# Performance work log

Measured on AMD Instinct MI355X. Metric: run time of the kernel, lower is better.

Reference implementation:

```python
import jax, jax.numpy as jnp
import numpy as np

B, XD, ZD, XE, H, NH = 8192, 4096, 1024, 64, 128, 4
NUM_STEPS, STEP, NOISE = 10, 0.01, 1.0
EPS = 1e-5


def setup_inputs() -> dict:
    key = jax.random.key(0)
    ks = jax.random.split(key, 16)
    w = lambda k, s: jax.random.normal(k, s, jnp.float32) * 0.02
    inp = {"x": jax.random.normal(ks[0], (B, XD), jnp.float32)}
    inp.update(
        px_W1=w(ks[1], (H, ZD)), px_b1=jnp.zeros(H, jnp.float32),
        px_W2=w(ks[2], (XD, H)), px_b2=jnp.zeros(XD, jnp.float32),
        emb_W=w(ks[3], (XE, XD)), emb_b=jnp.zeros(XE, jnp.float32),
        xp_W=w(ks[4], (H, XE)), xp_b=jnp.zeros(H, jnp.float32),
        zp_W=w(ks[5], (H, ZD)), zp_b=jnp.zeros(H, jnp.float32),
        sa_Wqkv=w(ks[6], (3 * H, H)), sa_bqkv=jnp.zeros(3 * H, jnp.float32),
        sa_Wo=w(ks[7], (H, H)), sa_bo=jnp.zeros(H, jnp.float32),
        ca_Wqkv=w(ks[8], (3 * H, H)), ca_bqkv=jnp.zeros(3 * H, jnp.float32),
        ca_Wo=w(ks[9], (H, H)), ca_bo=jnp.zeros(H, jnp.float32),
        ffn_W1=w(ks[10], (H, H)), ffn_b1=jnp.zeros(H, jnp.float32),
        ffn_W2=w(ks[11], (H, H)), ffn_b2=jnp.zeros(H, jnp.float32),
        ln1_g=jnp.ones(H, jnp.float32), ln1_b=jnp.zeros(H, jnp.float32),
        ln2_g=jnp.ones(H, jnp.float32), ln2_b=jnp.zeros(H, jnp.float32),
        ln3_g=jnp.ones(H, jnp.float32), ln3_b=jnp.zeros(H, jnp.float32),
        out_W=w(ks[12], (1, H)), out_b=jnp.zeros(1, jnp.float32),
    )
    return inp


def _ln(x, g, b):
    m = jnp.mean(x, -1, keepdims=True)
    v = jnp.var(x, -1, keepdims=True)
    return (x - m) * jax.lax.rsqrt(v + EPS) * g + b


def _mha(q, k, v, Wqkv, bqkv, Wo, bo):
    # torch nn.MultiheadAttention math, batch-first layout (B, S, E)
    E = q.shape[-1]
    d = E // NH
    Wq, Wk, Wv = jnp.split(Wqkv, 3, 0)
    bq, bk, bv = jnp.split(bqkv, 3, 0)
    hd = lambda t, W, bb: (t @ W.T + bb).reshape(t.shape[0], t.shape[1], NH, d)
    qh, kh, vh = hd(q, Wq, bq), hd(k, Wk, bk), hd(v, Wv, bv)
    s = jnp.einsum('bqhd,bkhd->bhqk', qh, kh) / jnp.sqrt(jnp.float32(d))
    a = jax.nn.softmax(s, -1)
    o = jnp.einsum('bhqk,bkhd->bqhd', a, vh).reshape(q.shape[0], q.shape[1], E)
    return o @ Wo.T + bo


def _forward(x, px_W1, px_b1, px_W2, px_b2, emb_W, emb_b, xp_W, xp_b, zp_W, zp_b,
             sa_Wqkv, sa_bqkv, sa_Wo, sa_bo, ca_Wqkv, ca_bqkv, ca_Wo, ca_bo,
             ffn_W1, ffn_b1, ffn_W2, ffn_b2, ln1_g, ln1_b, ln2_g, ln2_b,
             ln3_g, ln3_b, out_W, out_b):
    bsz = x.shape[0]
    px = lambda z: jax.nn.relu(z @ px_W1.T + px_b1) @ px_W2.T + px_b2
    grad_fn = jax.grad(lambda z: jnp.sum((px(z) - x) ** 2))
    ks = jax.random.split(jax.random.key(42), NUM_STEPS + 1)
    z0 = jax.random.normal(ks[0], (bsz, ZD), jnp.float32)

    def step(z, k):
        z = z - 0.5 * STEP * grad_fn(z)
        z = z + NOISE * jnp.sqrt(jnp.float32(STEP)) * jax.random.normal(k, z.shape, z.dtype)
        return z, None

    z, _ = jax.lax.scan(step, z0, ks[1:])
    z = jax.lax.stop_gradient(z)  # torch: z.detach()

    x_recon = px(z)                               # (B, XD)
    x_tok = (x @ emb_W.T + emb_b)[:, None, :]     # (B, 1, XE)
    z_lat = z[:, None, :]                         # (B, 1, ZD)
    x_h = x_tok @ xp_W.T + xp_b                   # (B, 1, H)
    z_h = z_lat @ zp_W.T + zp_b                   # (B, 1, H)
    sa = _mha(x_h, x_h, x_h, sa_Wqkv, sa_bqkv, sa_Wo, sa_bo)
    h1 = _ln(x_h + sa, ln1_g, ln1_b)
    ca = _mha(h1, z_h, z_h, ca_Wqkv, ca_bqkv, ca_Wo, ca_bo)
    h2 = _ln(h1 + ca, ln2_g, ln2_b)
    ff = jax.nn.relu(h2 @ ffn_W1.T + ffn_b1) @ ffn_W2.T + ffn_b2
    h3 = _ln(h2 + ff, ln3_g, ln3_b)
    y_pred = h3 @ out_W.T + out_b                 # (B, 1, 1)
    return x_recon, y_pred


def reference(x, px_W1, px_b1, px_W2, px_b2, emb_W, emb_b, xp_W, xp_b, zp_W, zp_b,
              sa_Wqkv, sa_bqkv, sa_Wo, sa_bo, ca_Wqkv, ca_bqkv, ca_Wo, ca_bo,
              ffn_W1, ffn_b1, ffn_W2, ffn_b2, ln1_g, ln1_b, ln2_g, ln2_b,
              ln3_g, ln3_b, out_W, out_b):
    return _forward(x, px_W1, px_b1, px_W2, px_b2, emb_W, emb_b, xp_W, xp_b,
                    zp_W, zp_b, sa_Wqkv, sa_bqkv, sa_Wo, sa_bo, ca_Wqkv,
                    ca_bqkv, ca_Wo, ca_bo, ffn_W1, ffn_b1, ffn_W2, ffn_b2,
                    ln1_g, ln1_b, ln2_g, ln2_b, ln3_g, ln3_b, out_W, out_b)
```

## Files before the change

kernel.cpp:

```cpp
#include <hip/hip_runtime.h>
#include <hip/hip_bf16.h>
#include <cstdint>
#include <cstddef>
#include <cmath>

#define B_     8192
#define XD_    4096
#define ZD_    1024
#define XE_    64
#define H_     128
#define ZN_    (B_*ZD_)

typedef __attribute__((ext_vector_type(8))) short short8_t;
typedef __attribute__((ext_vector_type(4))) float f32x4_t;
#define MFMA16(a,b,c) __builtin_amdgcn_mfma_f32_16x16x32_bf16((a),(b),(c),0,0,0)

__host__ __device__ __forceinline__ uint32_t rotl32_(uint32_t x, int r){ return (x<<r)|(x>>(32-r)); }

__host__ __device__ __forceinline__ void tf2x32(uint32_t k0, uint32_t k1,
                                                uint32_t x0, uint32_t x1,
                                                uint32_t* o0, uint32_t* o1){
  uint32_t k2 = k0 ^ k1 ^ 0x1BD11BDAu;
  x0 += k0; x1 += k1;
  x0 += x1; x1 = rotl32_(x1,13); x1 ^= x0;
  x0 += x1; x1 = rotl32_(x1,15); x1 ^= x0;
  x0 += x1; x1 = rotl32_(x1,26); x1 ^= x0;
  x0 += x1; x1 = rotl32_(x1, 6); x1 ^= x0;
  x0 += k1; x1 += k2 + 1u;
  x0 += x1; x1 = rotl32_(x1,17); x1 ^= x0;
  x0 += x1; x1 = rotl32_(x1,29); x1 ^= x0;
  x0 += x1; x1 = rotl32_(x1,16); x1 ^= x0;
  x0 += x1; x1 = rotl32_(x1,24); x1 ^= x0;
  x0 += k2; x1 += k0 + 2u;
  x0 += x1; x1 = rotl32_(x1,13); x1 ^= x0;
  x0 += x1; x1 = rotl32_(x1,15); x1 ^= x0;
  x0 += x1; x1 = rotl32_(x1,26); x1 ^= x0;
  x0 += x1; x1 = rotl32_(x1, 6); x1 ^= x0;
  x0 += k0; x1 += k1 + 3u;
  x0 += x1; x1 = rotl32_(x1,17); x1 ^= x0;
  x0 += x1; x1 = rotl32_(x1,29); x1 ^= x0;
  x0 += x1; x1 = rotl32_(x1,16); x1 ^= x0;
  x0 += x1; x1 = rotl32_(x1,24); x1 ^= x0;
  x0 += k1; x1 += k2 + 4u;
  x0 += x1; x1 = rotl32_(x1,13); x1 ^= x0;
  x0 += x1; x1 = rotl32_(x1,15); x1 ^= x0;
  x0 += x1; x1 = rotl32_(x1,26); x1 ^= x0;
  x0 += x1; x1 = rotl32_(x1, 6); x1 ^= x0;
  x0 += k2; x1 += k0 + 5u;
  *o0 = x0; *o1 = x1;
}

__device__ __forceinline__ float erfinv_(float x){
  float w = -__logf(fmaf(-x, x, 1.0f));
  float p;
  if (w < 5.0f){
    w -= 2.5f;
    p = 2.81022636e-08f;
    p = fmaf(p, w, 3.43273939e-07f);
    p = fmaf(p, w, -3.5233877e-06f);
    p = fmaf(p, w, -4.39150654e-06f);
    p = fmaf(p, w, 0.00021858087f);
    p = fmaf(p, w, -0.00125372503f);
    p = fmaf(p, w, -0.00417768164f);
    p = fmaf(p, w, 0.246640727f);
    p = fmaf(p, w, 1.50140941f);
  } else {
    w = sqrtf(w) - 3.0f;
    p = -0.000200214257f;
    p = fmaf(p, w, 0.000100950558f);
    p = fmaf(p, w, 0.00134934322f);
    p = fmaf(p, w, -0.00367342844f);
    p = fmaf(p, w, 0.00573950773f);
    p = fmaf(p, w, -0.0076224613f);
    p = fmaf(p, w, 0.00943887047f);
    p = fmaf(p, w, 1.00167406f);
    p = fmaf(p, w, 2.83297682f);
  }
  return p * x;
}

__device__ __forceinline__ float bits_to_normal(uint32_t bits){
  float f = __uint_as_float((bits >> 9) | 0x3f800000u) - 1.0f;
  float u = fmaxf(-0.99999994f, fmaf(f, 2.0f, -0.99999994f));
  return 1.41421356f * erfinv_(u);
}

__device__ __forceinline__ float rng_normal(uint32_t k0, uint32_t k1, uint32_t idx){
  uint32_t o0, o1; tf2x32(k0, k1, 0u, idx, &o0, &o1);
  return bits_to_normal(o0 ^ o1);
}

__device__ __forceinline__ ushort f2bf(float f){
  return __builtin_bit_cast(ushort, __float2bfloat16(f));
}
__device__ __forceinline__ float bf2f(ushort u){ return __uint_as_float(((uint32_t)u) << 16); }

__global__ void k_prepA(const float* __restrict__ saWo, const float* __restrict__ saWqkv,
                        const float* __restrict__ caWo, const float* __restrict__ caWqkv,
                        float* __restrict__ S, float* __restrict__ U){
  int blk = blockIdx.x, tid = threadIdx.x;
  int idx = (blk & 255) * 64 + tid;
  int i = idx >> 7, j = idx & 127;
  if (blk < 256){
    float acc = (i == j) ? 1.0f : 0.0f;
    for (int k = 0; k < H_; ++k) acc += saWo[i*H_ + k] * saWqkv[(2*H_ + k)*H_ + j];
    S[idx] = acc;
  } else {
    float acc = 0.0f;
    for (int k = 0; k < H_; ++k) acc += caWo[i*H_ + k] * caWqkv[(2*H_ + k)*H_ + j];
    U[idx] = acc;
  }
}

__global__ void k_prepB(const float* __restrict__ saWo, const float* __restrict__ sabqkv, const float* __restrict__ sabo,
                        const float* __restrict__ caWo, const float* __restrict__ cabqkv, const float* __restrict__ cabo,
                        const float* __restrict__ W2, const float* __restrict__ pb2,
                        float* __restrict__ s0, float* __restrict__ u0, float* __restrict__ cb,
                        uint32_t* __restrict__ dkeys){
  int blk = blockIdx.x, tid = threadIdx.x;
  if (blk == 0 && tid == 0){
    for (uint32_t i = 0; i < 11; ++i){
      uint32_t a, b; tf2x32(0u, 42u, 0u, i, &a, &b);
      dkeys[2*i] = a; dkeys[2*i+1] = b;
    }
  }
  if (blk < 2){
    int i = blk*64 + tid;
    float acc = sabo[i];
    for (int k = 0; k < H_; ++k) acc += saWo[i*H_ + k] * sabqkv[2*H_ + k];
    s0[i] = acc;
  } else if (blk < 4){
    int i = (blk-2)*64 + tid;
    float acc = cabo[i];
    for (int k = 0; k < H_; ++k) acc += caWo[i*H_ + k] * cabqkv[2*H_ + k];
    u0[i] = acc;
  } else {
    int j = (blk-4)*64 + tid;
    float acc = 0.0f;
    for (int c = 0; c < XD_; ++c) acc += pb2[c] * W2[(size_t)c*H_ + j];
    cb[j] = acc;
  }
}

__global__ void k_prepM(const float* __restrict__ W2, float* __restrict__ M){
  int idx = blockIdx.x*64 + threadIdx.x;
  int j1 = idx >> 7, j2 = idx & 127;
  float acc = 0.0f;
  for (int c = 0; c < XD_; ++c) acc += W2[(size_t)c*H_ + j1] * W2[(size_t)c*H_ + j2];
  M[idx] = acc;
}

__global__ void k_prepTR(const float* __restrict__ S, const float* __restrict__ U,
                         const float* __restrict__ xpW, const float* __restrict__ zpW,
                         const float* __restrict__ xpb, const float* __restrict__ zpb,
                         const float* __restrict__ s0, const float* __restrict__ u0,
                         float* __restrict__ T, float* __restrict__ R,
                         float* __restrict__ t0, float* __restrict__ r0v){
  int blk = blockIdx.x, tid = threadIdx.x;
  if (blk < 128){
    int idx = blk*64 + tid;
    int i = idx >> 6, e = idx & 63;
    float acc = 0.0f;
    for (int m = 0; m < H_; ++m) acc += S[i*H_ + m] * xpW[m*XE_ + e];
    T[idx] = acc;
  } else if (blk < 2176){
    int idx = (blk-128)*64 + tid;
    int i = idx >> 10, k = idx & 1023;
    float acc = 0.0f;
    for (int m = 0; m < H_; ++m) acc += U[i*H_ + m] * zpW[(size_t)m*ZD_ + k];
    R[idx] = acc;
  } else if (blk < 2178){
    int i = (blk-2176)*64 + tid;
    float acc = s0[i];
    for (int m = 0; m < H_; ++m) acc += S[i*H_ + m] * xpb[m];
    t0[i] = acc;
  } else {
    int i = (blk-2178)*64 + tid;
    float acc = u0[i];
    for (int m = 0; m < H_; ++m) acc += U[i*H_ + m] * zpb[m];
    r0v[i] = acc;
  }
}

__global__ void k_prepWXT(const float* __restrict__ W2, const float* __restrict__ T,
                          const float* __restrict__ embW, const float* __restrict__ embb,
                          const float* __restrict__ t0,
                          ushort* __restrict__ WXT, float* __restrict__ q0){
  int idx = blockIdx.x*256 + threadIdx.x;
  int j = idx >> 12, c = idx & 4095;
  float v;
  if (j < H_) v = W2[(size_t)c*H_ + j];
  else {
    int i = j - H_;
    float acc = 0.0f;
    for (int e = 0; e < XE_; ++e) acc += T[i*XE_ + e] * embW[(size_t)e*XD_ + c];
    v = acc;
  }
  WXT[idx] = f2bf(v);
  if (idx < H_){
    float acc = t0[idx];
    for (int e = 0; e < XE_; ++e) acc += T[idx*XE_ + e] * embb[e];
    q0[idx] = acc;
  }
}

__global__ void k_conv(const float* __restrict__ W2, const float* __restrict__ W1,
                       const float* __restrict__ Mm, const float* __restrict__ R,
                       ushort* __restrict__ W2bf, ushort* __restrict__ Mbf,
                       ushort* __restrict__ FBT){
  int idx = blockIdx.x*256 + threadIdx.x;
  if (idx < 524288) W2bf[idx] = f2bf(W2[idx]);
  else if (idx < 540672){ int i = idx - 524288; Mbf[i] = f2bf(2.0f*Mm[i]); }
  else { int i = idx - 540672; int j = i >> 10, k = i & 1023;
    FBT[i] = f2bf(j < H_ ? W1[j*ZD_ + k] : R[(size_t)(j-H_)*ZD_ + k]); }
}

__global__ void k_prepG(const float* __restrict__ W1, const float* __restrict__ R,
                        ushort* __restrict__ GGr){
  int idx = blockIdx.x*64 + threadIdx.x;
  int i = idx >> 7, k = idx & 127;
  float acc = 0.0f;
  if (i < 128){
    for (int m = 0; m < ZD_; ++m) acc += W1[(size_t)i*ZD_ + m] * W1[(size_t)k*ZD_ + m];
  } else {
    for (int m = 0; m < ZD_; ++m) acc += W1[(size_t)k*ZD_ + m] * R[(size_t)(i-128)*ZD_ + m];
  }
  GGr[idx] = f2bf(-0.005f * acc);
}

__global__ __launch_bounds__(256) void k_xpass_mfma(
    const float* __restrict__ x, const ushort* __restrict__ WXT,
    const float* __restrict__ cb, const float* __restrict__ q0,
    float* __restrict__ cneg, float* __restrict__ h1pre){
  __shared__ __align__(16) ushort xt[2][32*72];
  __shared__ __align__(16) ushort bt[2][128*72];
  const int t = threadIdx.x, lane = t & 63, w = t >> 6;
  const int bm = blockIdx.x >> 1, bn = blockIdx.x & 1;
  const int row0 = bm*32, ncol0 = bn*128;
  const int l15 = lane & 15, kq8 = (lane >> 4)*8, rq = (lane >> 4)*4;
  const int rt = w & 1, cb4 = (w >> 1)*4;
  const int xr = t >> 3, xk = (t & 7)*8;
  const int wn = t >> 1, wk = (t & 1)*32;
  f32x4_t acc[4] = {};
  {
    float4 v0 = *(const float4*)&x[(size_t)(row0+xr)*XD_ + xk];
    float4 v1 = *(const float4*)&x[(size_t)(row0+xr)*XD_ + xk + 4];
    union { ushort u[8]; uint4 q; } p;
    p.u[0]=f2bf(v0.x); p.u[1]=f2bf(v0.y); p.u[2]=f2bf(v0.z); p.u[3]=f2bf(v0.w);
    p.u[4]=f2bf(v1.x); p.u[5]=f2bf(v1.y); p.u[6]=f2bf(v1.z); p.u[7]=f2bf(v1.w);
    *(uint4*)&xt[0][xr*72 + xk] = p.q;
    const ushort* s = &WXT[(size_t)(ncol0+wn)*XD_ + wk];
    uint4 b0v=*(const uint4*)s, b1v=*(const uint4*)(s+8), b2v=*(const uint4*)(s+16), b3v=*(const uint4*)(s+24);
    ushort* d = &bt[0][wn*72 + wk];
    *(uint4*)d=b0v; *(uint4*)(d+8)=b1v; *(uint4*)(d+16)=b2v; *(uint4*)(d+24)=b3v;
  }
  float4 xv0, xv1; uint4 wb0, wb1, wb2, wb3;
  {
    xv0 = *(const float4*)&x[(size_t)(row0+xr)*XD_ + 64 + xk];
    xv1 = *(const float4*)&x[(size_t)(row0+xr)*XD_ + 64 + xk + 4];
    const ushort* s = &WXT[(size_t)(ncol0+wn)*XD_ + 64 + wk];
    wb0=*(const uint4*)s; wb1=*(const uint4*)(s+8); wb2=*(const uint4*)(s+16); wb3=*(const uint4*)(s+24);
  }
  #pragma unroll 1
  for (int it = 0; it < 64; ++it){
    __syncthreads();
    if (it < 63){
      union { ushort u[8]; uint4 q; } p;
      p.u[0]=f2bf(xv0.x); p.u[1]=f2bf(xv0.y); p.u[2]=f2bf(xv0.z); p.u[3]=f2bf(xv0.w);
      p.u[4]=f2bf(xv1.x); p.u[5]=f2bf(xv1.y); p.u[6]=f2bf(xv1.z); p.u[7]=f2bf(xv1.w);
      *(uint4*)&xt[(it+1)&1][xr*72 + xk] = p.q;
      ushort* d = &bt[(it+1)&1][wn*72 + wk];
      *(uint4*)d=wb0; *(uint4*)(d+8)=wb1; *(uint4*)(d+16)=wb2; *(uint4*)(d+24)=wb3;
    }
    if (it < 62){
      const int kt = (it+2)*64;
      xv0 = *(const float4*)&x[(size_t)(row0+xr)*XD_ + kt + xk];
      xv1 = *(const float4*)&x[(size_t)(row0+xr)*XD_ + kt + xk + 4];
      const ushort* s = &WXT[(size_t)(ncol0+wn)*XD_ + kt + wk];
      wb0=*(const uint4*)s; wb1=*(const uint4*)(s+8); wb2=*(const uint4*)(s+16); wb3=*(const uint4*)(s+24);
    }
    const ushort* xb = &xt[it&1][(rt*16+l15)*72];
    const ushort* bb = &bt[it&1][0];
    #pragma unroll
    for (int h = 0; h < 2; ++h){
      short8_t a = *(const short8_t*)(xb + h*32 + kq8);
      #pragma unroll
      for (int c = 0; c < 4; ++c){
        short8_t b = *(const short8_t*)(bb + ((cb4+c)*16+l15)*72 + h*32 + kq8);
        acc[c] = MFMA16(a, b, acc[c]);
      }
    }
  }
  #pragma unroll
  for (int c = 0; c < 4; ++c){
    int jl = (cb4+c)*16 + l15;
    #pragma unroll
    for (int r = 0; r < 4; ++r){
      int row = row0 + rt*16 + rq + r;
      float v = acc[c][r];
      if (bn == 0) cneg[(size_t)row*H_ + jl] = 2.0f*(cb[jl] - v);
      else         h1pre[(size_t)row*H_ + jl] = v + q0[jl];
    }
  }
}

__global__ __launch_bounds__(256) void k_noiseproj(
    const ushort* __restrict__ FBT, const uint32_t* __restrict__ dkeys,
    float* __restrict__ y0c0, ushort* __restrict__ NWR){
  __shared__ __align__(16) ushort at[64*72];
  const int t = threadIdx.x, lane = t & 63, w = t >> 6;
  const int l15 = lane & 15, kq8 = (lane >> 4)*8, rq = (lane >> 4)*4;
  const int p = blockIdx.x >> 7, mb = blockIdx.x & 127;
  const int gb0 = mb*64;
  const uint32_t k0 = dkeys[2*p], k1 = dkeys[2*p+1];
  const int arow = t >> 2, ak0 = (t & 3)*16;
  f32x4_t acc[16] = {};
  #pragma unroll 1
  for (int it = 0; it < 16; ++it){
    __syncthreads();
    {
      uint32_t base = (uint32_t)(gb0 + arow)*1024u + (uint32_t)(it*64 + ak0);
      union { ushort u[8]; uint4 q; } pk;
      #pragma unroll
      for (int j = 0; j < 8; ++j) pk.u[j] = f2bf(rng_normal(k0,k1,base+j));
      *(uint4*)&at[arow*72 + ak0] = pk.q;
      #pragma unroll
      for (int j = 0; j < 8; ++j) pk.u[j] = f2bf(rng_normal(k0,k1,base+8+j));
      *(uint4*)&at[arow*72 + ak0 + 8] = pk.q;
    }
    __syncthreads();
    #pragma unroll
    for (int h = 0; h < 2; ++h){
      short8_t a = *(const short8_t*)&at[(w*16+l15)*72 + h*32 + kq8];
      #pragma unroll
      for (int cf = 0; cf < 16; ++cf){
        short8_t b = *(const short8_t*)&FBT[(size_t)(cf*16+l15)*ZD_ + it*64 + h*32 + kq8];
        acc[cf] = MFMA16(a, b, acc[cf]);
      }
    }
  }
  #pragma unroll
  for (int cf = 0; cf < 16; ++cf){
    int col = cf*16 + l15;
    #pragma unroll
    for (int r = 0; r < 4; ++r){
      int row = gb0 + w*16 + rq + r;
      float v = acc[cf][r];
      if (p == 0) y0c0[(size_t)row*256 + col] = v;
      else NWR[(size_t)(p-1)*2097152 + (size_t)row*256 + col] = f2bf(0.1f*v);
    }
  }
}

__global__ __launch_bounds__(512) void k_lv2(
    const ushort* __restrict__ M2bf, const ushort* __restrict__ GGr,
    const float* __restrict__ y0c0, const ushort* __restrict__ NWR,
    const float* __restrict__ b1, const float* __restrict__ r0v,
    const float* __restrict__ cneg,
    ushort* __restrict__ hfin_bf, float* __restrict__ capre){
  __shared__ __align__(16) ushort abuf[16*136];
  __shared__ __align__(16) ushort glbuf[16*136];
  const int t = threadIdx.x, lane = t & 63, w = t >> 6;
  const int l15 = lane & 15, kq8 = (lane >> 4)*8, rq = (lane >> 4)*4;
  const int b0 = blockIdx.x * 16;
  const int myc = w*16 + l15;
  const int col2 = w*32 + l15;

  f32x4_t acc[2];
  #pragma unroll
  for (int nf = 0; nf < 2; ++nf)
    #pragma unroll
    for (int r = 0; r < 4; ++r)
      acc[nf][r] = y0c0[(size_t)(b0+rq+r)*256 + col2 + nf*16];
  float cn[4];
  #pragma unroll
  for (int r = 0; r < 4; ++r) cn[r] = cneg[(size_t)(b0+rq+r)*H_ + myc];
  float bb2[2];
  bb2[0] = (w < 4) ? b1[col2] : 0.0f;
  bb2[1] = (w < 4) ? b1[col2+16] : 0.0f;
  ushort nx[8];
  #pragma unroll
  for (int nf = 0; nf < 2; ++nf)
    #pragma unroll
    for (int r = 0; r < 4; ++r)
      nx[nf*4+r] = NWR[(size_t)(b0+rq+r)*256 + col2 + nf*16];

  #pragma unroll 1
  for (int s = 0; s < 10; ++s){
    if (w < 4){
      #pragma unroll
      for (int nf = 0; nf < 2; ++nf)
        #pragma unroll
        for (int r = 0; r < 4; ++r)
          abuf[(rq+r)*136 + col2 + nf*16] = f2bf(fmaxf(acc[nf][r] + bb2[nf], 0.0f));
    }
    __syncthreads();
    f32x4_t g2 = {};
    #pragma unroll
    for (int h = 0; h < 4; ++h){
      short8_t a = *(const short8_t*)&abuf[l15*136 + h*32 + kq8];
      short8_t b = *(const short8_t*)&M2bf[(size_t)myc*H_ + h*32 + kq8];
      g2 = MFMA16(a, b, g2);
// ... 145 lines not shown
  }
  x0 = h2a + fa; x1 = h2b + fbv;
  m = wsum64(x0 + x1) * (1.0f/128.0f);
  d0 = x0 - m; d1 = x1 - m;
  v = wsum64(d0*d0 + d1*d1) * (1.0f/128.0f);
  rs = rsqrtf(v + 1e-5f);
  float h3a = d0 * rs * ln3g[l]    + ln3b[l];
  float h3b = d1 * rs * ln3g[l+64] + ln3b[l+64];
  float py = wsum64(outW[l]*h3a + outW[l+64]*h3b);
  if (l == 0) y[b] = py + outb[0];
}

extern "C" void kernel_launch(void* const* d_in, const int* in_sizes, int n_in,
                              void* d_out, int out_size, void* d_ws, size_t ws_size,
                              hipStream_t stream){
  const float* x      = (const float*)d_in[0];
  const float* pxW1   = (const float*)d_in[1];
  const float* pxb1   = (const float*)d_in[2];
  const float* pxW2   = (const float*)d_in[3];
  const float* pxb2   = (const float*)d_in[4];
  const float* embW   = (const float*)d_in[5];
  const float* embb   = (const float*)d_in[6];
  const float* xpW    = (const float*)d_in[7];
  const float* xpb    = (const float*)d_in[8];
  const float* zpW    = (const float*)d_in[9];
  const float* zpb    = (const float*)d_in[10];
  const float* saWqkv = (const float*)d_in[11];
  const float* sabqkv = (const float*)d_in[12];
  const float* saWo   = (const float*)d_in[13];
  const float* sabo   = (const float*)d_in[14];
  const float* caWqkv = (const float*)d_in[15];
  const float* cabqkv = (const float*)d_in[16];
  const float* caWo   = (const float*)d_in[17];
  const float* cabo   = (const float*)d_in[18];
  const float* fW1    = (const float*)d_in[19];
  const float* fb1    = (const float*)d_in[20];
  const float* fW2    = (const float*)d_in[21];
  const float* fb2    = (const float*)d_in[22];
  const float* ln1g   = (const float*)d_in[23];
  const float* ln1b   = (const float*)d_in[24];
  const float* ln2g   = (const float*)d_in[25];
  const float* ln2b   = (const float*)d_in[26];
  const float* ln3g   = (const float*)d_in[27];
  const float* ln3b   = (const float*)d_in[28];
  const float* outW   = (const float*)d_in[29];
  const float* outb   = (const float*)d_in[30];
  (void)in_sizes; (void)n_in; (void)out_size; (void)ws_size;

  float* ws    = (float*)d_ws;
  float* cneg  = ws;
  float* h1pre = cneg + (size_t)B_*H_;
  float* capre = h1pre + (size_t)B_*H_;
  float* Rm    = capre + (size_t)B_*H_;
  float* Mm    = Rm + (size_t)H_*ZD_;
  float* Sm    = Mm + H_*H_;
  float* Um    = Sm + H_*H_;
  float* Tm    = Um + H_*H_;
  float* vs0   = Tm + H_*XE_;
  float* vu0   = vs0 + H_;
  float* vt0   = vu0 + H_;
  float* vq0   = vt0 + H_;
  float* vr0   = vq0 + H_;
  float* vcb   = vr0 + H_;
  uint32_t* dkeys = (uint32_t*)(vcb + H_);
  float* y0c0  = (float*)(dkeys + 32);
  ushort* WXT   = (ushort*)(y0c0 + (size_t)B_*256);
  ushort* W2bf  = WXT + (size_t)256*XD_;
  ushort* Mbf   = W2bf + (size_t)XD_*H_;
  ushort* FBT   = Mbf + H_*H_;
  ushort* GGr   = FBT + (size_t)256*ZD_;
  ushort* hfin  = GGr + (size_t)256*H_;
  ushort* NWR   = hfin + (size_t)B_*H_;

  float* xre   = (float*)d_out;
  float* ypred = xre + (size_t)B_*XD_;

  k_prepA   <<<512,  64, 0, stream>>>(saWo, saWqkv, caWo, caWqkv, Sm, Um);
  k_prepB   <<<6,    64, 0, stream>>>(saWo, sabqkv, sabo, caWo, cabqkv, cabo, pxW2, pxb2,
                                      vs0, vu0, vcb, dkeys);
  k_prepM   <<<256,  64, 0, stream>>>(pxW2, Mm);
  k_prepTR  <<<2180, 64, 0, stream>>>(Sm, Um, xpW, zpW, xpb, zpb, vs0, vu0, Tm, Rm, vt0, vr0);
  k_prepWXT <<<4096, 256, 0, stream>>>(pxW2, Tm, embW, embb, vt0, WXT, vq0);
  k_conv    <<<3136, 256, 0, stream>>>(pxW2, pxW1, Mm, Rm, W2bf, Mbf, FBT);
  k_prepG   <<<512,  64, 0, stream>>>(pxW1, Rm, GGr);
  k_noiseproj <<<1408, 256, 0, stream>>>(FBT, dkeys, y0c0, NWR);
  k_xpass_mfma <<<512, 256, 0, stream>>>(x, WXT, vcb, vq0, cneg, h1pre);
  k_lv2     <<<512, 512, 0, stream>>>(Mbf, GGr, y0c0, NWR, pxb1, vr0, cneg, hfin, capre);
  k_xrecon_mfma <<<4096, 256, 0, stream>>>(hfin, W2bf, pxb2, xre);
  k_tail    <<<2048, 256, 0, stream>>>(h1pre, capre, ln1g, ln1b, ln2g, ln2b, ln3g, ln3b,
                                       fW1, fb1, fW2, fb2, outW, outb, ypred);
}
```

Before: 900.2 us.

## Merge noise projection and x-pass GEMMs into one interleaved kernel

Two kernels are fused into one launch: the compute-bound RNG noise-projection GEMM and the memory-bound x-projection GEMM. Blocks are interleaved 11:4 so both kinds of work share the GPU at once and overlap. The noise-projection path also gets a double-buffered LDS tile, so the next RNG tile is generated while MFMAs run on the current one. The cost is a larger shared buffer for the noise blocks (sized for the x-pass), which may lower occupancy, plus higher register pressure from holding prefetched RNG values.

```diff
diff --git a/kernel.cpp b/kernel.cpp
--- a/kernel.cpp
+++ b/kernel.cpp
@@ -95,6 +95,14 @@
 }
 __device__ __forceinline__ float bf2f(ushort u){ return __uint_as_float(((uint32_t)u) << 16); }
 
+__device__ __forceinline__ void gen16(uint32_t k0, uint32_t k1, uint32_t base,
+                                      uint4* g0, uint4* g1){
+  union { ushort u[16]; uint4 q[2]; } pk;
+  #pragma unroll
+  for (int j = 0; j < 16; ++j) pk.u[j] = f2bf(rng_normal(k0,k1,base+(uint32_t)j));
+  *g0 = pk.q[0]; *g1 = pk.q[1];
+}
+
 __global__ void k_prepA(const float* __restrict__ saWo, const float* __restrict__ saWqkv,
                         const float* __restrict__ caWo, const float* __restrict__ caWqkv,
                         float* __restrict__ S, float* __restrict__ U){
@@ -228,126 +236,132 @@
   GGr[idx] = f2bf(-0.005f * acc);
 }
 
-__global__ __launch_bounds__(256) void k_xpass_mfma(
+__global__ __launch_bounds__(256) void k_npx(
+    const ushort* __restrict__ FBT, const uint32_t* __restrict__ dkeys,
+    float* __restrict__ y0c0, ushort* __restrict__ NWR,
     const float* __restrict__ x, const ushort* __restrict__ WXT,
-    const float* __restrict__ cb, const float* __restrict__ q0,
+    const float* __restrict__ cb, const float* __restrict__ q0v,
     float* __restrict__ cneg, float* __restrict__ h1pre){
-  __shared__ __align__(16) ushort xt[2][32*72];
-  __shared__ __align__(16) ushort bt[2][128*72];
-  const int t = threadIdx.x, lane = t & 63, w = t >> 6;
-  const int bm = blockIdx.x >> 1, bn = blockIdx.x & 1;
-  const int row0 = bm*32, ncol0 = bn*128;
-  const int l15 = lane & 15, kq8 = (lane >> 4)*8, rq = (lane >> 4)*4;
-  const int rt = w & 1, cb4 = (w >> 1)*4;
-  const int xr = t >> 3, xk = (t & 7)*8;
-  const int wn = t >> 1, wk = (t & 1)*32;
-  f32x4_t acc[4] = {};
-  {
-    float4 v0 = *(const float4*)&x[(size_t)(row0+xr)*XD_ + xk];
-    float4 v1 = *(const float4*)&x[(size_t)(row0+xr)*XD_ + xk + 4];
-    union { ushort u[8]; uint4 q; } p;
-    p.u[0]=f2bf(v0.x); p.u[1]=f2bf(v0.y); p.u[2]=f2bf(v0.z); p.u[3]=f2bf(v0.w);
-    p.u[4]=f2bf(v1.x); p.u[5]=f2bf(v1.y); p.u[6]=f2bf(v1.z); p.u[7]=f2bf(v1.w);
-    *(uint4*)&xt[0][xr*72 + xk] = p.q;
-    const ushort* s = &WXT[(size_t)(ncol0+wn)*XD_ + wk];
-    uint4 b0v=*(const uint4*)s, b1v=*(const uint4*)(s+8), b2v=*(const uint4*)(s+16), b3v=*(const uint4*)(s+24);
-    ushort* d = &bt[0][wn*72 + wk];
-    *(uint4*)d=b0v; *(uint4*)(d+8)=b1v; *(uint4*)(d+16)=b2v; *(uint4*)(d+24)=b3v;
-  }
-  float4 xv0, xv1; uint4 wb0, wb1, wb2, wb3;
-  {
-    xv0 = *(const float4*)&x[(size_t)(row0+xr)*XD_ + 64 + xk];
-    xv1 = *(const float4*)&x[(size_t)(row0+xr)*XD_ + 64 + xk + 4];
-    const ushort* s = &WXT[(size_t)(ncol0+wn)*XD_ + 64 + wk];
-    wb0=*(const uint4*)s; wb1=*(const uint4*)(s+8); wb2=*(const uint4*)(s+16); wb3=*(const uint4*)(s+24);
-  }
-  #pragma unroll 1
-  for (int it = 0; it < 64; ++it){
-    __syncthreads();
-    if (it < 63){
-      union { ushort u[8]; uint4 q; } p;
-      p.u[0]=f2bf(xv0.x); p.u[1]=f2bf(xv0.y); p.u[2]=f2bf(xv0.z); p.u[3]=f2bf(xv0.w);
-      p.u[4]=f2bf(xv1.x); p.u[5]=f2bf(xv1.y); p.u[6]=f2bf(xv1.z); p.u[7]=f2bf(xv1.w);
-      *(uint4*)&xt[(it+1)&1][xr*72 + xk] = p.q;
-      ushort* d = &bt[(it+1)&1][wn*72 + wk];
-      *(uint4*)d=wb0; *(uint4*)(d+8)=wb1; *(uint4*)(d+16)=wb2; *(uint4*)(d+24)=wb3;
-    }
-    if (it < 62){
-      const int kt = (it+2)*64;
-      xv0 = *(const float4*)&x[(size_t)(row0+xr)*XD_ + kt + xk];
-      xv1 = *(const float4*)&x[(size_t)(row0+xr)*XD_ + kt + xk + 4];
-      const ushort* s = &WXT[(size_t)(ncol0+wn)*XD_ + kt + wk];
-      wb0=*(const uint4*)s; wb1=*(const uint4*)(s+8); wb2=*(const uint4*)(s+16); wb3=*(const uint4*)(s+24);
-    }
-    const ushort* xb = &xt[it&1][(rt*16+l15)*72];
-    const ushort* bb = &bt[it&1][0];
-    #pragma unroll
-    for (int h = 0; h < 2; ++h){
-      short8_t a = *(const short8_t*)(xb + h*32 + kq8);
-      #pragma unroll
-      for (int c = 0; c < 4; ++c){
-        short8_t b = *(const short8_t*)(bb + ((cb4+c)*16+l15)*72 + h*32 + kq8);
-        acc[c] = MFMA16(a, b, acc[c]);
-      }
-    }
-  }
-  #pragma unroll
-  for (int c = 0; c < 4; ++c){
-    int jl = (cb4+c)*16 + l15;
-    #pragma unroll
-    for (int r = 0; r < 4; ++r){
-      int row = row0 + rt*16 + rq + r;
-      float v = acc[c][r];
-      if (bn == 0) cneg[(size_t)row*H_ + jl] = 2.0f*(cb[jl] - v);
-      else         h1pre[(size_t)row*H_ + jl] = v + q0[jl];
-    }
-  }
-}
-
-__global__ __launch_bounds__(256) void k_noiseproj(
-    const ushort* __restrict__ FBT, const uint32_t* __restrict__ dkeys,
-    float* __restrict__ y0c0, ushort* __restrict__ NWR){
-  __shared__ __align__(16) ushort at[64*72];
+  __shared__ __align__(16) ushort smem[23040];
   const int t = threadIdx.x, lane = t & 63, w = t >> 6;
   const int l15 = lane & 15, kq8 = (lane >> 4)*8, rq = (lane >> 4)*4;
-  const int p = blockIdx.x >> 7, mb = blockIdx.x & 127;
-  const int gb0 = mb*64;
-  const uint32_t k0 = dkeys[2*p], k1 = dkeys[2*p+1];
-  const int arow = t >> 2, ak0 = (t & 3)*16;
-  f32x4_t acc[16] = {};
-  #pragma unroll 1
-  for (int it = 0; it < 16; ++it){
+  const int grp = blockIdx.x / 15, rem = blockIdx.x % 15;
+
+  if (rem < 11){
+    ushort* at0 = smem;
+    ushort* at1 = smem + 4608;
+    const int np = grp*11 + rem;
+    const int p = np >> 7, mb = np & 127;
+    const int gb0 = mb*64;
+    const uint32_t k0 = dkeys[2*p], k1 = dkeys[2*p+1];
+    const int arow = t >> 2, ak0 = (t & 3)*16;
+    const uint32_t rbase = (uint32_t)(gb0 + arow)*1024u + (uint32_t)ak0;
+    f32x4_t acc[16] = {};
+    uint4 g0, g1;
+    gen16(k0, k1, rbase, &g0, &g1);
+    { ushort* d = at0 + arow*72 + ak0; *(uint4*)d = g0; *(uint4*)(d+8) = g1; }
     __syncthreads();
+    #pragma unroll 1
+    for (int it = 0; it < 16; ++it){
+      if (it < 15) gen16(k0, k1, rbase + (uint32_t)((it+1)*64), &g0, &g1);
+      const ushort* ab = ((it & 1) ? at1 : at0) + (w*16 + l15)*72;
+      #pragma unroll
+      for (int h = 0; h < 2; ++h){
+        short8_t a = *(const short8_t*)(ab + h*32 + kq8);
+        #pragma unroll
+        for (int cf = 0; cf < 16; ++cf){
+          short8_t b = *(const short8_t*)&FBT[(size_t)(cf*16+l15)*ZD_ + it*64 + h*32 + kq8];
+          acc[cf] = MFMA16(a, b, acc[cf]);
+        }
+      }
+      if (it < 15){
+        ushort* d = ((it & 1) ? at0 : at1) + arow*72 + ak0;
+        *(uint4*)d = g0; *(uint4*)(d+8) = g1;
+      }
+      __syncthreads();
+    }
+    #pragma unroll
+    for (int cf = 0; cf < 16; ++cf){
+      int col = cf*16 + l15;
+      #pragma unroll
+      for (int r = 0; r < 4; ++r){
+        int row = gb0 + w*16 + rq + r;
+        float v = acc[cf][r];
+        if (p == 0) y0c0[(size_t)row*256 + col] = v;
+        else NWR[(size_t)(p-1)*2097152 + (size_t)row*256 + col] = f2bf(0.1f*v);
+      }
+    }
+  } else {
+    ushort* xt0 = smem;
+    ushort* xt1 = smem + 2304;
+    ushort* bt0 = smem + 4608;
+    ushort* bt1 = smem + 13824;
+    const int xp = grp*4 + (rem - 11);
+    const int bm = xp >> 1, bn = xp & 1;
+    const int row0 = bm*32, ncol0 = bn*128;
+    const int rt = w & 1, cb4 = (w >> 1)*4;
+    const int xr = t >> 3, xk = (t & 7)*8;
+    const int wn = t >> 1, wk = (t & 1)*32;
+    f32x4_t acc[4] = {};
     {
-      uint32_t base = (uint32_t)(gb0 + arow)*1024u + (uint32_t)(it*64 + ak0);
-      union { ushort u[8]; uint4 q; } pk;
-      #pragma unroll
-      for (int j = 0; j < 8; ++j) pk.u[j] = f2bf(rng_normal(k0,k1,base+j));
-      *(uint4*)&at[arow*72 + ak0] = pk.q;
-      #pragma unroll
-      for (int j = 0; j < 8; ++j) pk.u[j] = f2bf(rng_normal(k0,k1,base+8+j));
-      *(uint4*)&at[arow*72 + ak0 + 8] = pk.q;
-    }
-    __syncthreads();
-    #pragma unroll
-    for (int h = 0; h < 2; ++h){
-      short8_t a = *(const short8_t*)&at[(w*16+l15)*72 + h*32 + kq8];
-      #pragma unroll
-      for (int cf = 0; cf < 16; ++cf){
-        short8_t b = *(const short8_t*)&FBT[(size_t)(cf*16+l15)*ZD_ + it*64 + h*32 + kq8];
-        acc[cf] = MFMA16(a, b, acc[cf]);
-      }
-    }
-  }
-  #pragma unroll
-  for (int cf = 0; cf < 16; ++cf){
-    int col = cf*16 + l15;
-    #pragma unroll
-    for (int r = 0; r < 4; ++r){
-      int row = gb0 + w*16 + rq + r;
-      float v = acc[cf][r];
-      if (p == 0) y0c0[(size_t)row*256 + col] = v;
-      else NWR[(size_t)(p-1)*2097152 + (size_t)row*256 + col] = f2bf(0.1f*v);
+      float4 v0 = *(const float4*)&x[(size_t)(row0+xr)*XD_ + xk];
+      float4 v1 = *(const float4*)&x[(size_t)(row0+xr)*XD_ + xk + 4];
+      union { ushort u[8]; uint4 q; } p;
+      p.u[0]=f2bf(v0.x); p.u[1]=f2bf(v0.y); p.u[2]=f2bf(v0.z); p.u[3]=f2bf(v0.w);
+      p.u[4]=f2bf(v1.x); p.u[5]=f2bf(v1.y); p.u[6]=f2bf(v1.z); p.u[7]=f2bf(v1.w);
+      *(uint4*)&xt0[xr*72 + xk] = p.q;
+      const ushort* s = &WXT[(size_t)(ncol0+wn)*XD_ + wk];
+      uint4 b0v=*(const uint4*)s, b1v=*(const uint4*)(s+8), b2v=*(const uint4*)(s+16), b3v=*(const uint4*)(s+24);
+      ushort* d = &bt0[wn*72 + wk];
+      *(uint4*)d=b0v; *(uint4*)(d+8)=b1v; *(uint4*)(d+16)=b2v; *(uint4*)(d+24)=b3v;
+    }
+    float4 xv0, xv1; uint4 wb0, wb1, wb2, wb3;
+    {
+      xv0 = *(const float4*)&x[(size_t)(row0+xr)*XD_ + 64 + xk];
+      xv1 = *(const float4*)&x[(size_t)(row0+xr)*XD_ + 64 + xk + 4];
+      const ushort* s = &WXT[(size_t)(ncol0+wn)*XD_ + 64 + wk];
+      wb0=*(const uint4*)s; wb1=*(const uint4*)(s+8); wb2=*(const uint4*)(s+16); wb3=*(const uint4*)(s+24);
+    }
+    #pragma unroll 1
+    for (int it = 0; it < 64; ++it){
+      __syncthreads();
+      if (it < 63){
+        union { ushort u[8]; uint4 q; } p;
+        p.u[0]=f2bf(xv0.x); p.u[1]=f2bf(xv0.y); p.u[2]=f2bf(xv0.z); p.u[3]=f2bf(xv0.w);
+        p.u[4]=f2bf(xv1.x); p.u[5]=f2bf(xv1.y); p.u[6]=f2bf(xv1.z); p.u[7]=f2bf(xv1.w);
+        *(uint4*)&(((it+1)&1) ? xt1 : xt0)[xr*72 + xk] = p.q;
+        ushort* d = &(((it+1)&1) ? bt1 : bt0)[wn*72 + wk];
+        *(uint4*)d=wb0; *(uint4*)(d+8)=wb1; *(uint4*)(d+16)=wb2; *(uint4*)(d+24)=wb3;
+      }
+      if (it < 62){
+        const int kt = (it+2)*64;
+        xv0 = *(const float4*)&x[(size_t)(row0+xr)*XD_ + kt + xk];
+        xv1 = *(const float4*)&x[(size_t)(row0+xr)*XD_ + kt + xk + 4];
+        const ushort* s = &WXT[(size_t)(ncol0+wn)*XD_ + kt + wk];
+        wb0=*(const uint4*)s; wb1=*(const uint4*)(s+8); wb2=*(const uint4*)(s+16); wb3=*(const uint4*)(s+24);
+      }
+      const ushort* xb = &((it&1) ? xt1 : xt0)[(rt*16+l15)*72];
+      const ushort* bb = (it&1) ? bt1 : bt0;
+      #pragma unroll
+      for (int h = 0; h < 2; ++h){
+        short8_t a = *(const short8_t*)(xb + h*32 + kq8);
+        #pragma unroll
+        for (int c = 0; c < 4; ++c){
+          short8_t b = *(const short8_t*)(bb + ((cb4+c)*16+l15)*72 + h*32 + kq8);
+          acc[c] = MFMA16(a, b, acc[c]);
+        }
+      }
+    }
+    #pragma unroll
+    for (int c = 0; c < 4; ++c){
+      int jl = (cb4+c)*16 + l15;
+      #pragma unroll
+      for (int r = 0; r < 4; ++r){
+        int row = row0 + rt*16 + rq + r;
+        float v = acc[c][r];
+        if (bn == 0) cneg[(size_t)row*H_ + jl] = 2.0f*(cb[jl] - v);
+        else         h1pre[(size_t)row*H_ + jl] = v + q0v[jl];
+      }
     }
   }
 }
@@ -630,8 +644,7 @@
   k_prepWXT <<<4096, 256, 0, stream>>>(pxW2, Tm, embW, embb, vt0, WXT, vq0);
   k_conv    <<<3136, 256, 0, stream>>>(pxW2, pxW1, Mm, Rm, W2bf, Mbf, FBT);
   k_prepG   <<<512,  64, 0, stream>>>(pxW1, Rm, GGr);
-  k_noiseproj <<<1408, 256, 0, stream>>>(FBT, dkeys, y0c0, NWR);
-  k_xpass_mfma <<<512, 256, 0, stream>>>(x, WXT, vcb, vq0, cneg, h1pre);
+  k_npx     <<<1920, 256, 0, stream>>>(FBT, dkeys, y0c0, NWR, x, WXT, vcb, vq0, cneg, h1pre);
   k_lv2     <<<512, 512, 0, stream>>>(Mbf, GGr, y0c0, NWR, pxb1, vr0, cneg, hfin, capre);
   k_xrecon_mfma <<<4096, 256, 0, stream>>>(hfin, W2bf, pxb2, xre);
   k_tail    <<<2048, 256, 0, stream>>>(h1pre, capre, ln1g, ln1b, ln2g, ln2b, ln3g, ln3b,
```

After: 943.4 us. 1.05x slower.

## Double-buffer RNG tile in noise projection and split columns across 8 waves

Applied to the files above, without the earlier changes.

The noise-projection kernel now runs 512 threads: 8 waves split both rows and the 256 output columns, so each thread generates 8 normals per step instead of 16 and keeps 8 accumulators instead of 16. The LDS tile is double-buffered, and the next tile's RNG values are generated during the current step's MFMAs, with one barrier per iteration instead of two. The rotate in the Threefry hash uses a rotate builtin on device. The aim is to hide RNG cost behind matrix math and cut register pressure; the cost is more LDS per block and the larger block size changing occupancy.

```diff
diff --git a/kernel.cpp b/kernel.cpp
--- a/kernel.cpp
+++ b/kernel.cpp
@@ -15,7 +15,13 @@
 typedef __attribute__((ext_vector_type(4))) float f32x4_t;
 #define MFMA16(a,b,c) __builtin_amdgcn_mfma_f32_16x16x32_bf16((a),(b),(c),0,0,0)
 
-__host__ __device__ __forceinline__ uint32_t rotl32_(uint32_t x, int r){ return (x<<r)|(x>>(32-r)); }
+__host__ __device__ __forceinline__ uint32_t rotl32_(uint32_t x, int r){
+#ifdef __HIP_DEVICE_COMPILE__
+  return __builtin_rotateleft32(x, (uint32_t)r);
+#else
+  return (x<<r)|(x>>(32-r));
+#endif
+}
 
 __host__ __device__ __forceinline__ void tf2x32(uint32_t k0, uint32_t k1,
                                                 uint32_t x0, uint32_t x1,
@@ -95,6 +101,13 @@
 }
 __device__ __forceinline__ float bf2f(ushort u){ return __uint_as_float(((uint32_t)u) << 16); }
 
+__device__ __forceinline__ void gen8(uint32_t k0, uint32_t k1, uint32_t base, uint4* g){
+  union { ushort u[8]; uint4 q; } pk;
+  #pragma unroll
+  for (int j = 0; j < 8; ++j) pk.u[j] = f2bf(rng_normal(k0,k1,base+(uint32_t)j));
+  *g = pk.q;
+}
+
 __global__ void k_prepA(const float* __restrict__ saWo, const float* __restrict__ saWqkv,
                         const float* __restrict__ caWo, const float* __restrict__ caWqkv,
                         float* __restrict__ S, float* __restrict__ U){
@@ -228,6 +241,52 @@
   GGr[idx] = f2bf(-0.005f * acc);
 }
 
+__global__ __launch_bounds__(512) void k_noiseproj(
+    const ushort* __restrict__ FBT, const uint32_t* __restrict__ dkeys,
+    float* __restrict__ y0c0, ushort* __restrict__ NWR){
+  __shared__ __align__(16) ushort at[2][64*72];
+  const int t = threadIdx.x, lane = t & 63, w = t >> 6;
+  const int l15 = lane & 15, kq8 = (lane >> 4)*8, rq = (lane >> 4)*4;
+  const int p = blockIdx.x >> 7, mb = blockIdx.x & 127;
+  const int gb0 = mb*64;
+  const uint32_t k0 = dkeys[2*p], k1 = dkeys[2*p+1];
+  const int wr = w & 3, wc = w >> 2;
+  const int arow = t >> 3, ak0 = (t & 7)*8;
+  const uint32_t rbase = (uint32_t)(gb0 + arow)*1024u + (uint32_t)ak0;
+  f32x4_t acc[8] = {};
+  uint4 g;
+  gen8(k0, k1, rbase, &g);
+  *(uint4*)&at[0][arow*72 + ak0] = g;
+  __syncthreads();
+  #pragma unroll 1
+  for (int it = 0; it < 16; ++it){
+    if (it < 15) gen8(k0, k1, rbase + (uint32_t)((it+1)*64), &g);
+    const ushort* ab = at[it&1] + (wr*16 + l15)*72;
+    #pragma unroll
+    for (int h = 0; h < 2; ++h){
+      short8_t a = *(const short8_t*)(ab + h*32 + kq8);
+      #pragma unroll
+      for (int cf = 0; cf < 8; ++cf){
+        short8_t b = *(const short8_t*)&FBT[(size_t)(wc*128 + cf*16 + l15)*ZD_ + it*64 + h*32 + kq8];
+        acc[cf] = MFMA16(a, b, acc[cf]);
+      }
+    }
+    if (it < 15) *(uint4*)&at[(it+1)&1][arow*72 + ak0] = g;
+    __syncthreads();
+  }
+  #pragma unroll
+  for (int cf = 0; cf < 8; ++cf){
+    int col = wc*128 + cf*16 + l15;
+    #pragma unroll
+    for (int r = 0; r < 4; ++r){
+      int row = gb0 + wr*16 + rq + r;
+      float v = acc[cf][r];
+      if (p == 0) y0c0[(size_t)row*256 + col] = v;
+      else NWR[(size_t)(p-1)*2097152 + (size_t)row*256 + col] = f2bf(0.1f*v);
+    }
+  }
+}
+
 __global__ __launch_bounds__(256) void k_xpass_mfma(
     const float* __restrict__ x, const ushort* __restrict__ WXT,
     const float* __restrict__ cb, const float* __restrict__ q0,
@@ -300,54 +359,6 @@
       float v = acc[c][r];
       if (bn == 0) cneg[(size_t)row*H_ + jl] = 2.0f*(cb[jl] - v);
       else         h1pre[(size_t)row*H_ + jl] = v + q0[jl];
-    }
-  }
-}
-
-__global__ __launch_bounds__(256) void k_noiseproj(
-    const ushort* __restrict__ FBT, const uint32_t* __restrict__ dkeys,
-    float* __restrict__ y0c0, ushort* __restrict__ NWR){
-  __shared__ __align__(16) ushort at[64*72];
-  const int t = threadIdx.x, lane = t & 63, w = t >> 6;
-  const int l15 = lane & 15, kq8 = (lane >> 4)*8, rq = (lane >> 4)*4;
-  const int p = blockIdx.x >> 7, mb = blockIdx.x & 127;
-  const int gb0 = mb*64;
-  const uint32_t k0 = dkeys[2*p], k1 = dkeys[2*p+1];
-  const int arow = t >> 2, ak0 = (t & 3)*16;
-  f32x4_t acc[16] = {};
-  #pragma unroll 1
-  for (int it = 0; it < 16; ++it){
-    __syncthreads();
-    {
-      uint32_t base = (uint32_t)(gb0 + arow)*1024u + (uint32_t)(it*64 + ak0);
-      union { ushort u[8]; uint4 q; } pk;
-      #pragma unroll
-      for (int j = 0; j < 8; ++j) pk.u[j] = f2bf(rng_normal(k0,k1,base+j));
-      *(uint4*)&at[arow*72 + ak0] = pk.q;
-      #pragma unroll
-      for (int j = 0; j < 8; ++j) pk.u[j] = f2bf(rng_normal(k0,k1,base+8+j));
-      *(uint4*)&at[arow*72 + ak0 + 8] = pk.q;
-    }
-    __syncthreads();
-    #pragma unroll
-    for (int h = 0; h < 2; ++h){
-      short8_t a = *(const short8_t*)&at[(w*16+l15)*72 + h*32 + kq8];
-      #pragma unroll
-      for (int cf = 0; cf < 16; ++cf){
-        short8_t b = *(const short8_t*)&FBT[(size_t)(cf*16+l15)*ZD_ + it*64 + h*32 + kq8];
-        acc[cf] = MFMA16(a, b, acc[cf]);
-      }
-    }
-  }
-  #pragma unroll
-  for (int cf = 0; cf < 16; ++cf){
-    int col = cf*16 + l15;
-    #pragma unroll
-    for (int r = 0; r < 4; ++r){
-      int row = gb0 + w*16 + rq + r;
-      float v = acc[cf][r];
-      if (p == 0) y0c0[(size_t)row*256 + col] = v;
-      else NWR[(size_t)(p-1)*2097152 + (size_t)row*256 + col] = f2bf(0.1f*v);
     }
   }
 }
@@ -630,7 +641,7 @@
   k_prepWXT <<<4096, 256, 0, stream>>>(pxW2, Tm, embW, embb, vt0, WXT, vq0);
   k_conv    <<<3136, 256, 0, stream>>>(pxW2, pxW1, Mm, Rm, W2bf, Mbf, FBT);
   k_prepG   <<<512,  64, 0, stream>>>(pxW1, Rm, GGr);
-  k_noiseproj <<<1408, 256, 0, stream>>>(FBT, dkeys, y0c0, NWR);
+  k_noiseproj <<<1408, 512, 0, stream>>>(FBT, dkeys, y0c0, NWR);
   k_xpass_mfma <<<512, 256, 0, stream>>>(x, WXT, vcb, vq0, cneg, h1pre);
   k_lv2     <<<512, 512, 0, stream>>>(Mbf, GGr, y0c0, NWR, pxb1, vr0, cneg, hfin, capre);
   k_xrecon_mfma <<<4096, 256, 0, stream>>>(hfin, W2bf, pxb2, xre);
```

Measured after the change: 955.2 us. 6.1% more time.

## Split-K weight Gram preps, merge G into conv, and make noise projection LDS-free

Applied to the files above, without the earlier changes.

The Gram matrices M (W2ᵀW2 over 4096) and G (over 1024) were computed by tiny 64-thread kernels with long serial loops. They are now computed as 8-way split-K partials in one wide kernel and reduced inside the conversion kernel, which drops the separate prepM and prepG launches. The noise projection kernel now has each wave generate its own 16-row A fragment straight into registers, with no shared memory or barriers, and the grid is remapped to one 16-row tile per wave. It also uses a hardware rotate builtin on device. The cost is extra partial-sum workspace and an added reduction pass.

```diff
diff --git a/kernel.cpp b/kernel.cpp
--- a/kernel.cpp
+++ b/kernel.cpp
@@ -15,7 +15,13 @@
 typedef __attribute__((ext_vector_type(4))) float f32x4_t;
 #define MFMA16(a,b,c) __builtin_amdgcn_mfma_f32_16x16x32_bf16((a),(b),(c),0,0,0)
 
-__host__ __device__ __forceinline__ uint32_t rotl32_(uint32_t x, int r){ return (x<<r)|(x>>(32-r)); }
+__host__ __device__ __forceinline__ uint32_t rotl32_(uint32_t x, int r){
+#ifdef __HIP_DEVICE_COMPILE__
+  return __builtin_rotateleft32(x, (uint32_t)r);
+#else
+  return (x<<r)|(x>>(32-r));
+#endif
+}
 
 __host__ __device__ __forceinline__ void tf2x32(uint32_t k0, uint32_t k1,
                                                 uint32_t x0, uint32_t x1,
@@ -95,6 +101,13 @@
 }
 __device__ __forceinline__ float bf2f(ushort u){ return __uint_as_float(((uint32_t)u) << 16); }
 
+__device__ __forceinline__ void gen8(uint32_t k0, uint32_t k1, uint32_t base, uint4* g){
+  union { ushort u[8]; uint4 q; } pk;
+  #pragma unroll
+  for (int j = 0; j < 8; ++j) pk.u[j] = f2bf(rng_normal(k0,k1,base+(uint32_t)j));
+  *g = pk.q;
+}
+
 __global__ void k_prepA(const float* __restrict__ saWo, const float* __restrict__ saWqkv,
                         const float* __restrict__ caWo, const float* __restrict__ caWqkv,
                         float* __restrict__ S, float* __restrict__ U){
@@ -140,14 +153,6 @@
     for (int c = 0; c < XD_; ++c) acc += pb2[c] * W2[(size_t)c*H_ + j];
     cb[j] = acc;
   }
-}
-
-__global__ void k_prepM(const float* __restrict__ W2, float* __restrict__ M){
-  int idx = blockIdx.x*64 + threadIdx.x;
-  int j1 = idx >> 7, j2 = idx & 127;
-  float acc = 0.0f;
-  for (int c = 0; c < XD_; ++c) acc += W2[(size_t)c*H_ + j1] * W2[(size_t)c*H_ + j2];
-  M[idx] = acc;
 }
 
 __global__ void k_prepTR(const float* __restrict__ S, const float* __restrict__ U,
@@ -182,6 +187,35 @@
   }
 }
 
+__global__ void k_prepMG_part(const float* __restrict__ W2, const float* __restrict__ W1,
+                              const float* __restrict__ R,
+                              float* __restrict__ Mpart, float* __restrict__ Gpart){
+  int gid = blockIdx.x*256 + threadIdx.x;
+  if (gid < 131072){
+    int slice = gid >> 14, i = gid & 16383;
+    int j1 = i >> 7, j2 = i & 127;
+    int c0 = slice*512;
+    float acc = 0.0f;
+    for (int c = c0; c < c0+512; ++c)
+      acc += W2[(size_t)c*H_ + j1] * W2[(size_t)c*H_ + j2];
+    Mpart[(size_t)slice*16384 + i] = acc;
+  } else {
+    int g = gid - 131072;
+    int slice = g >> 15, i2 = g & 32767;
+    int i = i2 >> 7, k = i2 & 127;
+    int m0 = slice*128;
+    float acc = 0.0f;
+    if (i < 128){
+      for (int m = m0; m < m0+128; ++m)
+        acc += W1[(size_t)i*ZD_ + m] * W1[(size_t)k*ZD_ + m];
+    } else {
+      for (int m = m0; m < m0+128; ++m)
+        acc += W1[(size_t)k*ZD_ + m] * R[(size_t)(i-128)*ZD_ + m];
+    }
+    Gpart[(size_t)slice*32768 + i2] = acc;
+  }
+}
+
 __global__ void k_prepWXT(const float* __restrict__ W2, const float* __restrict__ T,
                           const float* __restrict__ embW, const float* __restrict__ embb,
                           const float* __restrict__ t0,
@@ -205,27 +239,71 @@
 }
 
 __global__ void k_conv(const float* __restrict__ W2, const float* __restrict__ W1,
-                       const float* __restrict__ Mm, const float* __restrict__ R,
+                       const float* __restrict__ R,
+                       const float* __restrict__ Mpart, const float* __restrict__ Gpart,
                        ushort* __restrict__ W2bf, ushort* __restrict__ Mbf,
-                       ushort* __restrict__ FBT){
+                       ushort* __restrict__ FBT, ushort* __restrict__ GGr){
   int idx = blockIdx.x*256 + threadIdx.x;
   if (idx < 524288) W2bf[idx] = f2bf(W2[idx]);
-  else if (idx < 540672){ int i = idx - 524288; Mbf[i] = f2bf(2.0f*Mm[i]); }
-  else { int i = idx - 540672; int j = i >> 10, k = i & 1023;
-    FBT[i] = f2bf(j < H_ ? W1[j*ZD_ + k] : R[(size_t)(j-H_)*ZD_ + k]); }
-}
-
-__global__ void k_prepG(const float* __restrict__ W1, const float* __restrict__ R,
-                        ushort* __restrict__ GGr){
-  int idx = blockIdx.x*64 + threadIdx.x;
-  int i = idx >> 7, k = idx & 127;
-  float acc = 0.0f;
-  if (i < 128){
-    for (int m = 0; m < ZD_; ++m) acc += W1[(size_t)i*ZD_ + m] * W1[(size_t)k*ZD_ + m];
+  else if (idx < 540672){
+    int i = idx - 524288;
+    float s = 0.0f;
+    #pragma unroll
+    for (int p = 0; p < 8; ++p) s += Mpart[(size_t)p*16384 + i];
+    Mbf[i] = f2bf(2.0f*s);
+  } else if (idx < 802816){
+    int i = idx - 540672; int j = i >> 10, k = i & 1023;
+    FBT[i] = f2bf(j < H_ ? W1[j*ZD_ + k] : R[(size_t)(j-H_)*ZD_ + k]);
   } else {
-    for (int m = 0; m < ZD_; ++m) acc += W1[(size_t)k*ZD_ + m] * R[(size_t)(i-128)*ZD_ + m];
-  }
-  GGr[idx] = f2bf(-0.005f * acc);
+    int i = idx - 802816;
+    float s = 0.0f;
+    #pragma unroll
+    for (int p = 0; p < 8; ++p) s += Gpart[(size_t)p*32768 + i];
+    GGr[i] = f2bf(-0.005f*s);
+  }
+}
+
+__global__ __launch_bounds__(256) void k_noiseproj(
+    const ushort* __restrict__ FBT, const uint32_t* __restrict__ dkeys,
+    float* __restrict__ y0c0, ushort* __restrict__ NWR){
+  const int t = threadIdx.x, lane = t & 63, w = t >> 6;
+  const int l15 = lane & 15, kq8 = (lane >> 4)*8, rq = (lane >> 4)*4;
+  const int gwid = blockIdx.x*4 + w;
+  const int p = gwid >> 9, mb = gwid & 511;
+  const int row0 = mb*16;
+  const uint32_t k0 = dkeys[2*p], k1 = dkeys[2*p+1];
+  const uint32_t rbase = (uint32_t)(row0 + l15)*1024u + (uint32_t)kq8;
+  f32x4_t acc[16] = {};
+  #pragma unroll 1
+  for (int it = 0; it < 16; ++it){
+    uint4 g0, g1;
+    gen8(k0, k1, rbase + (uint32_t)(it*64), &g0);
+    gen8(k0, k1, rbase + (uint32_t)(it*64 + 32), &g1);
+    short8_t a0 = __builtin_bit_cast(short8_t, g0);
+    short8_t a1 = __builtin_bit_cast(short8_t, g1);
+    const ushort* fb = &FBT[(size_t)l15*ZD_ + it*64 + kq8];
+    #pragma unroll
+    for (int cf = 0; cf < 16; ++cf){
+      short8_t b0 = *(const short8_t*)(fb + (size_t)cf*16*ZD_);
+      acc[cf] = MFMA16(a0, b0, acc[cf]);
+    }
+    #pragma unroll
+    for (int cf = 0; cf < 16; ++cf){
+      short8_t b1 = *(const short8_t*)(fb + (size_t)cf*16*ZD_ + 32);
+      acc[cf] = MFMA16(a1, b1, acc[cf]);
+    }
+  }
+  #pragma unroll
+  for (int cf = 0; cf < 16; ++cf){
+    int col = cf*16 + l15;
+    #pragma unroll
+    for (int r = 0; r < 4; ++r){
+      int row = row0 + rq + r;
+      float v = acc[cf][r];
+      if (p == 0) y0c0[(size_t)row*256 + col] = v;
+      else NWR[(size_t)(p-1)*2097152 + (size_t)row*256 + col] = f2bf(0.1f*v);
+    }
+  }
 }
 
 __global__ __launch_bounds__(256) void k_xpass_mfma(
@@ -300,54 +378,6 @@
       float v = acc[c][r];
       if (bn == 0) cneg[(size_t)row*H_ + jl] = 2.0f*(cb[jl] - v);
       else         h1pre[(size_t)row*H_ + jl] = v + q0[jl];
-    }
-  }
-}
-
-__global__ __launch_bounds__(256) void k_noiseproj(
-    const ushort* __restrict__ FBT, const uint32_t* __restrict__ dkeys,
-    float* __restrict__ y0c0, ushort* __restrict__ NWR){
-  __shared__ __align__(16) ushort at[64*72];
-  const int t = threadIdx.x, lane = t & 63, w = t >> 6;
-  const int l15 = lane & 15, kq8 = (lane >> 4)*8, rq = (lane >> 4)*4;
-  const int p = blockIdx.x >> 7, mb = blockIdx.x & 127;
-  const int gb0 = mb*64;
-  const uint32_t k0 = dkeys[2*p], k1 = dkeys[2*p+1];
-  const int arow = t >> 2, ak0 = (t & 3)*16;
-  f32x4_t acc[16] = {};
-  #pragma unroll 1
-  for (int it = 0; it < 16; ++it){
-    __syncthreads();
-    {
-      uint32_t base = (uint32_t)(gb0 + arow)*1024u + (uint32_t)(it*64 + ak0);
-      union { ushort u[8]; uint4 q; } pk;
-      #pragma unroll
-      for (int j = 0; j < 8; ++j) pk.u[j] = f2bf(rng_normal(k0,k1,base+j));
-      *(uint4*)&at[arow*72 + ak0] = pk.q;
-      #pragma unroll
-      for (int j = 0; j < 8; ++j) pk.u[j] = f2bf(rng_normal(k0,k1,base+8+j));
-      *(uint4*)&at[arow*72 + ak0 + 8] = pk.q;
-    }
-    __syncthreads();
-    #pragma unroll
-    for (int h = 0; h < 2; ++h){
-      short8_t a = *(const short8_t*)&at[(w*16+l15)*72 + h*32 + kq8];
-      #pragma unroll
-      for (int cf = 0; cf < 16; ++cf){
-        short8_t b = *(const short8_t*)&FBT[(size_t)(cf*16+l15)*ZD_ + it*64 + h*32 + kq8];
-        acc[cf] = MFMA16(a, b, acc[cf]);
-      }
-    }
-  }
-  #pragma unroll
-  for (int cf = 0; cf < 16; ++cf){
-    int col = cf*16 + l15;
-    #pragma unroll
-    for (int r = 0; r < 4; ++r){
-      int row = gb0 + w*16 + rq + r;
-      float v = acc[cf][r];
-      if (p == 0) y0c0[(size_t)row*256 + col] = v;
-      else NWR[(size_t)(p-1)*2097152 + (size_t)row*256 + col] = f2bf(0.1f*v);
     }
   }
 }
@@ -599,8 +629,7 @@
   float* h1pre = cneg + (size_t)B_*H_;
   float* capre = h1pre + (size_t)B_*H_;
   float* Rm    = capre + (size_t)B_*H_;
-  float* Mm    = Rm + (size_t)H_*ZD_;
-  float* Sm    = Mm + H_*H_;
+  float* Sm    = Rm + (size_t)H_*ZD_;
   float* Um    = Sm + H_*H_;
   float* Tm    = Um + H_*H_;
   float* vs0   = Tm + H_*XE_;
@@ -609,7 +638,9 @@
   float* vq0   = vt0 + H_;
   float* vr0   = vq0 + H_;
   float* vcb   = vr0 + H_;
-  uint32_t* dkeys = (uint32_t*)(vcb + H_);
+  float* Mpart = vcb + H_;
+  float* Gpart = Mpart + 131072;
+  uint32_t* dkeys = (uint32_t*)(Gpart + 262144);
   float* y0c0  = (float*)(dkeys + 32);
   ushort* WXT   = (ushort*)(y0c0 + (size_t)B_*256);
   ushort* W2bf  = WXT + (size_t)256*XD_;
@@ -625,11 +656,10 @@
   k_prepA   <<<512,  64, 0, stream>>>(saWo, saWqkv, caWo, caWqkv, Sm, Um);
   k_prepB   <<<6,    64, 0, stream>>>(saWo, sabqkv, sabo, caWo, cabqkv, cabo, pxW2, pxb2,
                                       vs0, vu0, vcb, dkeys);
-  k_prepM   <<<256,  64, 0, stream>>>(pxW2, Mm);
   k_prepTR  <<<2180, 64, 0, stream>>>(Sm, Um, xpW, zpW, xpb, zpb, vs0, vu0, Tm, Rm, vt0, vr0);
+  k_prepMG_part <<<1536, 256, 0, stream>>>(pxW2, pxW1, Rm, Mpart, Gpart);
   k_prepWXT <<<4096, 256, 0, stream>>>(pxW2, Tm, embW, embb, vt0, WXT, vq0);
-  k_conv    <<<3136, 256, 0, stream>>>(pxW2, pxW1, Mm, Rm, W2bf, Mbf, FBT);
-  k_prepG   <<<512,  64, 0, stream>>>(pxW1, Rm, GGr);
+  k_conv    <<<3264, 256, 0, stream>>>(pxW2, pxW1, Rm, Mpart, Gpart, W2bf, Mbf, FBT, GGr);
   k_noiseproj <<<1408, 256, 0, stream>>>(FBT, dkeys, y0c0, NWR);
   k_xpass_mfma <<<512, 256, 0, stream>>>(x, WXT, vcb, vq0, cneg, h1pre);
   k_lv2     <<<512, 512, 0, stream>>>(Mbf, GGr, y0c0, NWR, pxb1, vr0, cneg, hfin, capre);
```

Result: slower. 933.4 us (+3.7%).
